# Kernel tuning notes

Hardware: AMD Instinct MI355X
Metric: run time of the kernel (lower is better)

## Reference

```python
import jax, jax.numpy as jnp
import numpy as np

D_MODEL = 768
KAN_HIDDEN = 2048
NUM_CP = 16        # number of B-spline control points / coefficients per edge
DEGREE = 3         # cubic splines
RMIN, RMAX = -4.0, 4.0


def bspline_basis(x, num_cp=NUM_CP, degree=DEGREE, rmin=RMIN, rmax=RMAX):
    """Cox-de Boor B-spline basis.
    x: (N, D) -> basis: (N, D, num_cp). Uniform knots extended by `degree`
    on each side so that [rmin, rmax] has full basis support.
    """
    h = (rmax - rmin) / (num_cp - degree)
    # K = num_cp + degree + 1 knots
    knots = rmin - degree * h + jnp.arange(num_cp + degree + 1, dtype=x.dtype) * h
    xe = x[..., None]  # (N, D, 1)
    # degree-0 indicator bases: (N, D, num_cp + degree)
    b = ((xe >= knots[:-1]) & (xe < knots[1:])).astype(x.dtype)
    for d in range(1, degree + 1):
        t0 = knots[:-(d + 1)]   # t[k]
        t1 = knots[d:-1]        # t[k+d]
        t2 = knots[d + 1:]      # t[k+d+1]
        t3 = knots[1:-d]        # t[k+1]
        b = (xe - t0) / (t1 - t0) * b[..., :-1] + (t2 - xe) / (t2 - t3) * b[..., 1:]
    return b  # (N, D, num_cp)


def kan_layer(x, w):
    """x: (N, Din); w: (Dout, Din, num_cp) per-edge spline coefficients."""
    basis = bspline_basis(x)                      # (N, Din, K)
    return jnp.einsum('ndk,odk->no', basis, w)    # (N, Dout)


def setup_inputs() -> dict:
    key = jax.random.key(0)
    kx, k1, k2 = jax.random.split(key, 3)
    x = jax.random.normal(kx, (2, 2048, D_MODEL), dtype=jnp.float32)
    # spline coefficient tables, small init like nn.init scaled normal
    w1 = jax.random.normal(k1, (KAN_HIDDEN, D_MODEL, NUM_CP), dtype=jnp.float32) * (1.0 / np.sqrt(D_MODEL * NUM_CP))
    w2 = jax.random.normal(k2, (D_MODEL, KAN_HIDDEN, NUM_CP), dtype=jnp.float32) * (1.0 / np.sqrt(KAN_HIDDEN * NUM_CP))
    return {"x": x, "w1": w1, "w2": w2}


def reference(x, w1, w2):
    B, T, D = x.shape
    input_dtype = x.dtype
    h = x.reshape(B * T, D).astype(jnp.float32)
    h = kan_layer(h, w1)                # (B*T, KAN_HIDDEN)
    h = kan_layer(h, w2)                # (B*T, D_MODEL)
    h = h.astype(input_dtype)
    # dropout p=0.0 / eval mode -> identity
    return h.reshape(B, T, -1)
```

## Files before the change

### kernel.cpp

```cpp
#include <hip/hip_runtime.h>
#include <stdint.h>

typedef __attribute__((ext_vector_type(8))) short short8;
typedef __attribute__((ext_vector_type(4))) float f32x4;
typedef __attribute__((ext_vector_type(4))) int i32x4;

#define DMODEL 768
#define HID    2048
#define MROWS  4096

#define KINVH  (13.0f/8.0f)
#define KNOT0  (-4.0f - 3.0f*(8.0f/13.0f))

__device__ __forceinline__ unsigned short f2bf(float f) {
  unsigned int u = __float_as_uint(f);
  unsigned int r = (u + 0x7FFFu + ((u >> 16) & 1u)) >> 16;
  return (unsigned short)r;
}

template<int DIN>
__global__ void __launch_bounds__(256) conv_pack(const float* __restrict__ src,
                                                 unsigned short* __restrict__ dst,
                                                 int total_waves) {
  constexpr int NK2 = DIN / 2;
  int gw = blockIdx.x * 4 + (threadIdx.x >> 6);
  if (gw >= total_waves) return;
  int l   = threadIdx.x & 63;
  int cb  = gw / NK2;
  int kt2 = gw % NK2;
  int c16 = l & 15, q = l >> 4;
  int col = cb * 16 + c16;
  const float* s = src + ((size_t)col * DIN + kt2 * 2 + (q >> 1)) * 16 + (q & 1) * 8;
  float4 v0 = *(const float4*)s;
  float4 v1 = *(const float4*)(s + 4);
  short8 o;
  o[0] = (short)f2bf(v0.x); o[1] = (short)f2bf(v0.y);
  o[2] = (short)f2bf(v0.z); o[3] = (short)f2bf(v0.w);
  o[4] = (short)f2bf(v1.x); o[5] = (short)f2bf(v1.y);
  o[6] = (short)f2bf(v1.z); o[7] = (short)f2bf(v1.w);
  unsigned short* d = dst + (((size_t)cb * NK2 + kt2) * 64 + q * 16 + c16) * 8;
  *(short8*)d = o;
}

__global__ void __launch_bounds__(256) reduce2(float4* __restrict__ p, int n4) {
  int i = blockIdx.x * 256 + threadIdx.x;
  if (i >= n4) return;
  float4 a = p[i], b = p[i + n4];
  float4 r;
  r.x = a.x + b.x; r.y = a.y + b.y; r.z = a.z + b.z; r.w = a.w + b.w;
  p[i] = r;
}

__global__ void __launch_bounds__(256) reduce4(const float4* __restrict__ p,
                                               float4* __restrict__ out, int n4) {
  int i = blockIdx.x * 256 + threadIdx.x;
  if (i >= n4) return;
  float4 a = p[i], b = p[i + n4], c = p[i + 2 * n4], d = p[i + 3 * n4];
  float4 r;
  r.x = a.x + b.x + c.x + d.x;
  r.y = a.y + b.y + c.y + d.y;
  r.z = a.z + b.z + c.z + d.z;
  r.w = a.w + b.w + c.w + d.w;
  out[i] = r;
}

template<int DIN, int DOUT, int SPLITK>
__global__ void __launch_bounds__(256, 4)
kan_gemm(const float* __restrict__ X, const unsigned short* __restrict__ Wb,
         float* __restrict__ Out) {
  constexpr int BM  = 64;
  constexpr int BN  = 256;
  constexpr int NK  = (DIN * 16) / 64;
  constexpr int NK2 = DIN / 2;
  constexpr int NKS = NK / SPLITK;
  constexpr int GX  = MROWS / BM;
  constexpr int GY  = DOUT / BN;
  constexpr int CPX = (GX * GY) / 8;
  __shared__ __align__(16) char smA[BM * 128];

  const int tid  = threadIdx.x;
  const int lane = tid & 63;
  const int wid  = tid >> 6;

  const int d    = blockIdx.x + blockIdx.y * GX;
  const int lf   = (d & 7) * CPX + (d >> 3);
  const int brow = (lf % GX) * BM;
  const int bcol = (lf / GX) * BN;
  const int kt0  = blockIdx.z * NKS;
  const int kt1  = kt0 + NKS;

  f32x4 acc[4][4];
#pragma unroll
  for (int m = 0; m < 4; ++m)
#pragma unroll
    for (int n = 0; n < 4; ++n) acc[m][n] = (f32x4){0.f, 0.f, 0.f, 0.f};

  int a_base[4], a_sw[4];
#pragma unroll
  for (int m = 0; m < 4; ++m) {
    int row   = m * 16 + (lane & 15);
    a_base[m] = row * 128 + ((lane >> 4) * 16);
    a_sw[m]   = (row & 7) << 4;
  }

  const unsigned short* bp[4];
#pragma unroll
  for (int n = 0; n < 4; ++n)
    bp[n] = Wb + ((size_t)(bcol / 16 + wid * 4 + n) * NK2 + (size_t)kt0 * 2) * 512
               + lane * 8;

  const int br_ = tid >> 2;
  const int bd_ = tid & 3;
  const float* xrow = X + (size_t)(brow + br_) * DIN + bd_;

  float xcur = xrow[(size_t)kt0 * 4];
  short8 bv[2][4];
#pragma unroll
  for (int n = 0; n < 4; ++n) {
    bv[0][n] = *(const short8*)(bp[n]);
    bv[1][n] = *(const short8*)(bp[n] + 512);
    bp[n] += 1024;
  }

  for (int kt = kt0; kt < kt1; ++kt) {
    __syncthreads();

    {
      float u  = (xcur - KNOT0) * KINVH;
      float uf = floorf(u);
      int   jj = (int)uf;
      float t  = u - uf;
      float t2 = t * t, t3 = t2 * t;
      float p0 = (1.0f / 6.0f) * (1.0f - 3.0f * t + 3.0f * t2 - t3);
      float p1 = (1.0f / 6.0f) * (4.0f - 6.0f * t2 + 3.0f * t3);
      float p2 = (1.0f / 6.0f) * (1.0f + 3.0f * t + 3.0f * t2 - 3.0f * t3);
      float p3 = (1.0f / 6.0f) * t3;

      int base = br_ * 128 + bd_ * 32;
      int sw   = (br_ & 7) << 4;
      *(i32x4*)(smA + (base ^ sw))        = (i32x4){0, 0, 0, 0};
      *(i32x4*)(smA + ((base + 16) ^ sw)) = (i32x4){0, 0, 0, 0};
      unsigned short q0 = f2bf(p0), q1 = f2bf(p1), q2 = f2bf(p2), q3 = f2bf(p3);
      int k0 = jj - 3;
      if ((unsigned)(k0 + 0) < 16u) *(unsigned short*)(smA + ((base + (k0 + 0) * 2) ^ sw)) = q0;
      if ((unsigned)(k0 + 1) < 16u) *(unsigned short*)(smA + ((base + (k0 + 1) * 2) ^ sw)) = q1;
      if ((unsigned)(k0 + 2) < 16u) *(unsigned short*)(smA + ((base + (k0 + 2) * 2) ^ sw)) = q2;
      if ((unsigned)(k0 + 3) < 16u) *(unsigned short*)(smA + ((base + (k0 + 3) * 2) ^ sw)) = q3;
    }

    {
      int ktn = (kt + 1 < kt1) ? kt + 1 : kt;
      xcur = xrow[(size_t)ktn * 4];
    }

    __syncthreads();

#pragma unroll
    for (int kk = 0; kk < 2; ++kk) {
      short8 a[4];
#pragma unroll
      for (int m = 0; m < 4; ++m)
        a[m] = *(const short8*)(smA + ((a_base[m] + kk * 64) ^ a_sw[m]));
#pragma unroll
      for (int m = 0; m < 4; ++m)
#pragma unroll
        for (int n = 0; n < 4; ++n)
          acc[m][n] = __builtin_amdgcn_mfma_f32_16x16x32_bf16(a[m], bv[kk][n], acc[m][n], 0, 0, 0);
    }

    if (kt + 1 < kt1) {
#pragma unroll
      for (int n = 0; n < 4; ++n) {
        bv[0][n] = *(const short8*)(bp[n]);
        bv[1][n] = *(const short8*)(bp[n] + 512);
        bp[n] += 1024;
      }
    }
  }

  float* outp = Out + (size_t)blockIdx.z * MROWS * DOUT;
#pragma unroll
  for (int m = 0; m < 4; ++m)
#pragma unroll
    for (int n = 0; n < 4; ++n)
#pragma unroll
      for (int q = 0; q < 4; ++q) {
        int grow = brow + m * 16 + (lane >> 4) * 4 + q;
        int gcol = bcol + wid * 64 + n * 16 + (lane & 15);
        outp[(size_t)grow * DOUT + gcol] = acc[m][n][q];
      }
}

extern "C" void kernel_launch(void* const* d_in, const int* in_sizes, int n_in,
                              void* d_out, int out_size, void* d_ws, size_t ws_size,
                              hipStream_t stream) {
  const float* x  = (const float*)d_in[0];
  const float* w1 = (const float*)d_in[1];
  const float* w2 = (const float*)d_in[2];
  float* out = (float*)d_out;

  char* ws = (char*)d_ws;
  unsigned short* wgb   = (unsigned short*)ws;
  float*          part1 = (float*)(ws + 50331648);
  float*          hbf   = part1;
  float*          part2 = (float*)(ws + 83886080);

  {
    const int waves = (HID / 16) * (DMODEL / 2);
    conv_pack<DMODEL><<<waves / 4, 256, 0, stream>>>(w1, wgb, waves);
  }
  kan_gemm<DMODEL, HID, 2>
      <<<dim3(MROWS / 64, HID / 256, 2), 256, 0, stream>>>(x, wgb, part1);
  const int hn4 = (MROWS * HID) / 4;
  reduce2<<<hn4 / 256, 256, 0, stream>>>((float4*)part1, hn4);

  {
    const int waves = (DMODEL / 16) * (HID / 2);
    conv_pack<HID><<<waves / 4, 256, 0, stream>>>(w2, wgb, waves);
  }
  kan_gemm<HID, DMODEL, 4>
      <<<dim3(MROWS / 64, DMODEL / 256, 4), 256, 0, stream>>>(hbf, wgb, part2);
  const int rn4 = (MROWS * DMODEL) / 4;
  reduce4<<<rn4 / 256, 256, 0, stream>>>((const float4*)part2, (float4*)out, rn4);
}
```

Before: 454.5 us.

## Fuse w2 packing with hidden reduce, narrow second GEMM tile, simplify basis math

Merges the w2 bf16 packing and the split-K reduction of the first layer into one launch, which removes a kernel launch and lets the two memory-bound jobs run side by side. The GEMM tile width becomes a template parameter, and the second layer now uses BN=128, doubling its grid to fill more CUs. The cubic B-spline weights are rewritten in the (1-t) form with fewer operations, and bf16 conversion now calls the HIP intrinsic. Narrower tiles reuse each A tile less, so more basis rebuilding and X reads happen per output.

```diff
diff --git a/kernel.cpp b/kernel.cpp
--- a/kernel.cpp
+++ b/kernel.cpp
@@ -1,4 +1,5 @@
 #include <hip/hip_runtime.h>
+#include <hip/hip_bf16.h>
 #include <stdint.h>
 
 typedef __attribute__((ext_vector_type(8))) short short8;
@@ -13,18 +14,14 @@
 #define KNOT0  (-4.0f - 3.0f*(8.0f/13.0f))
 
 __device__ __forceinline__ unsigned short f2bf(float f) {
-  unsigned int u = __float_as_uint(f);
-  unsigned int r = (u + 0x7FFFu + ((u >> 16) & 1u)) >> 16;
-  return (unsigned short)r;
+  __hip_bfloat16 h = __float2bfloat16(f);
+  return *reinterpret_cast<unsigned short*>(&h);
 }
 
 template<int DIN>
-__global__ void __launch_bounds__(256) conv_pack(const float* __restrict__ src,
-                                                 unsigned short* __restrict__ dst,
-                                                 int total_waves) {
+__device__ __forceinline__ void pack_wave(const float* __restrict__ src,
+                                          unsigned short* __restrict__ dst, int gw) {
   constexpr int NK2 = DIN / 2;
-  int gw = blockIdx.x * 4 + (threadIdx.x >> 6);
-  if (gw >= total_waves) return;
   int l   = threadIdx.x & 63;
   int cb  = gw / NK2;
   int kt2 = gw % NK2;
@@ -38,17 +35,30 @@
   o[2] = (short)f2bf(v0.z); o[3] = (short)f2bf(v0.w);
   o[4] = (short)f2bf(v1.x); o[5] = (short)f2bf(v1.y);
   o[6] = (short)f2bf(v1.z); o[7] = (short)f2bf(v1.w);
-  unsigned short* d = dst + (((size_t)cb * NK2 + kt2) * 64 + q * 16 + c16) * 8;
-  *(short8*)d = o;
-}
-
-__global__ void __launch_bounds__(256) reduce2(float4* __restrict__ p, int n4) {
-  int i = blockIdx.x * 256 + threadIdx.x;
-  if (i >= n4) return;
-  float4 a = p[i], b = p[i + n4];
-  float4 r;
-  r.x = a.x + b.x; r.y = a.y + b.y; r.z = a.z + b.z; r.w = a.w + b.w;
-  p[i] = r;
+  *(short8*)(dst + (((size_t)cb * NK2 + kt2) * 64 + q * 16 + c16) * 8) = o;
+}
+
+__global__ void __launch_bounds__(256) conv_pack1(const float* __restrict__ src,
+                                                  unsigned short* __restrict__ dst) {
+  pack_wave<DMODEL>(src, dst, blockIdx.x * 4 + (threadIdx.x >> 6));
+}
+
+__global__ void __launch_bounds__(256) pack2_reduce2(const float* __restrict__ w2,
+                                                     unsigned short* __restrict__ dst,
+                                                     float4* __restrict__ p, int n4) {
+  constexpr int PACK_BLOCKS = ((DMODEL / 16) * (HID / 2)) / 4;
+  int b = blockIdx.x;
+  if (b < PACK_BLOCKS) {
+    pack_wave<HID>(w2, dst, b * 4 + (threadIdx.x >> 6));
+  } else {
+    int i = (b - PACK_BLOCKS) * 256 + threadIdx.x;
+    if (i < n4) {
+      float4 a = p[i], q = p[i + n4];
+      float4 r;
+      r.x = a.x + q.x; r.y = a.y + q.y; r.z = a.z + q.z; r.w = a.w + q.w;
+      p[i] = r;
+    }
+  }
 }
 
 __global__ void __launch_bounds__(256) reduce4(const float4* __restrict__ p,
@@ -64,12 +74,12 @@
   out[i] = r;
 }
 
-template<int DIN, int DOUT, int SPLITK>
+template<int DIN, int DOUT, int BN, int SPLITK>
 __global__ void __launch_bounds__(256, 4)
 kan_gemm(const float* __restrict__ X, const unsigned short* __restrict__ Wb,
          float* __restrict__ Out) {
   constexpr int BM  = 64;
-  constexpr int BN  = 256;
+  constexpr int FN  = BN / 64;
   constexpr int NK  = (DIN * 16) / 64;
   constexpr int NK2 = DIN / 2;
   constexpr int NKS = NK / SPLITK;
@@ -89,11 +99,11 @@
   const int kt0  = blockIdx.z * NKS;
   const int kt1  = kt0 + NKS;
 
-  f32x4 acc[4][4];
+  f32x4 acc[4][FN];
 #pragma unroll
   for (int m = 0; m < 4; ++m)
 #pragma unroll
-    for (int n = 0; n < 4; ++n) acc[m][n] = (f32x4){0.f, 0.f, 0.f, 0.f};
+    for (int n = 0; n < FN; ++n) acc[m][n] = (f32x4){0.f, 0.f, 0.f, 0.f};
 
   int a_base[4], a_sw[4];
 #pragma unroll
@@ -103,10 +113,10 @@
     a_sw[m]   = (row & 7) << 4;
   }
 
-  const unsigned short* bp[4];
-#pragma unroll
-  for (int n = 0; n < 4; ++n)
-    bp[n] = Wb + ((size_t)(bcol / 16 + wid * 4 + n) * NK2 + (size_t)kt0 * 2) * 512
+  const unsigned short* bp[FN];
+#pragma unroll
+  for (int n = 0; n < FN; ++n)
+    bp[n] = Wb + ((size_t)(bcol / 16 + wid * FN + n) * NK2 + (size_t)kt0 * 2) * 512
                + lane * 8;
 
   const int br_ = tid >> 2;
@@ -114,9 +124,9 @@
   const float* xrow = X + (size_t)(brow + br_) * DIN + bd_;
 
   float xcur = xrow[(size_t)kt0 * 4];
-  short8 bv[2][4];
-#pragma unroll
-  for (int n = 0; n < 4; ++n) {
+  short8 bv[2][FN];
+#pragma unroll
+  for (int n = 0; n < FN; ++n) {
     bv[0][n] = *(const short8*)(bp[n]);
     bv[1][n] = *(const short8*)(bp[n] + 512);
     bp[n] += 1024;
@@ -130,11 +140,13 @@
       float uf = floorf(u);
       int   jj = (int)uf;
       float t  = u - uf;
+      float s1 = 1.0f - t;
       float t2 = t * t, t3 = t2 * t;
-      float p0 = (1.0f / 6.0f) * (1.0f - 3.0f * t + 3.0f * t2 - t3);
-      float p1 = (1.0f / 6.0f) * (4.0f - 6.0f * t2 + 3.0f * t3);
-      float p2 = (1.0f / 6.0f) * (1.0f + 3.0f * t + 3.0f * t2 - 3.0f * t3);
-      float p3 = (1.0f / 6.0f) * t3;
+      float s2 = s1 * s1, s3 = s2 * s1;
+      float p0 = s3 * (1.0f / 6.0f);
+      float p3 = t3 * (1.0f / 6.0f);
+      float p1 = fmaf(0.5f, t3, 2.0f / 3.0f) - t2;
+      float p2 = fmaf(0.5f, s3, 2.0f / 3.0f) - s2;
 
       int base = br_ * 128 + bd_ * 32;
       int sw   = (br_ & 7) << 4;
@@ -164,13 +176,13 @@
 #pragma unroll
       for (int m = 0; m < 4; ++m)
 #pragma unroll
-        for (int n = 0; n < 4; ++n)
+        for (int n = 0; n < FN; ++n)
           acc[m][n] = __builtin_amdgcn_mfma_f32_16x16x32_bf16(a[m], bv[kk][n], acc[m][n], 0, 0, 0);
     }
 
     if (kt + 1 < kt1) {
 #pragma unroll
-      for (int n = 0; n < 4; ++n) {
+      for (int n = 0; n < FN; ++n) {
         bv[0][n] = *(const short8*)(bp[n]);
         bv[1][n] = *(const short8*)(bp[n] + 512);
         bp[n] += 1024;
@@ -182,11 +194,11 @@
 #pragma unroll
   for (int m = 0; m < 4; ++m)
 #pragma unroll
-    for (int n = 0; n < 4; ++n)
+    for (int n = 0; n < FN; ++n)
 #pragma unroll
       for (int q = 0; q < 4; ++q) {
         int grow = brow + m * 16 + (lane >> 4) * 4 + q;
-        int gcol = bcol + wid * 64 + n * 16 + (lane & 15);
+        int gcol = bcol + wid * (BN / 4) + n * 16 + (lane & 15);
         outp[(size_t)grow * DOUT + gcol] = acc[m][n][q];
       }
 }
@@ -205,21 +217,18 @@
   float*          hbf   = part1;
   float*          part2 = (float*)(ws + 83886080);
 
+  conv_pack1<<<((HID / 16) * (DMODEL / 2)) / 4, 256, 0, stream>>>(w1, wgb);
+  kan_gemm<DMODEL, HID, 256, 2>
+      <<<dim3(MROWS / 64, HID / 256, 2), 256, 0, stream>>>(x, wgb, part1);
+
   {
-    const int waves = (HID / 16) * (DMODEL / 2);
-    conv_pack<DMODEL><<<waves / 4, 256, 0, stream>>>(w1, wgb, waves);
-  }
-  kan_gemm<DMODEL, HID, 2>
-      <<<dim3(MROWS / 64, HID / 256, 2), 256, 0, stream>>>(x, wgb, part1);
-  const int hn4 = (MROWS * HID) / 4;
-  reduce2<<<hn4 / 256, 256, 0, stream>>>((float4*)part1, hn4);
-
-  {
-    const int waves = (DMODEL / 16) * (HID / 2);
-    conv_pack<HID><<<waves / 4, 256, 0, stream>>>(w2, wgb, waves);
-  }
-  kan_gemm<HID, DMODEL, 4>
-      <<<dim3(MROWS / 64, DMODEL / 256, 4), 256, 0, stream>>>(hbf, wgb, part2);
+    const int hn4 = (MROWS * HID) / 4;
+    const int packB = ((DMODEL / 16) * (HID / 2)) / 4;
+    const int redB  = hn4 / 256;
+    pack2_reduce2<<<packB + redB, 256, 0, stream>>>(w2, wgb, (float4*)part1, hn4);
+  }
+  kan_gemm<HID, DMODEL, 128, 4>
+      <<<dim3(MROWS / 64, DMODEL / 128, 4), 256, 0, stream>>>(hbf, wgb, part2);
   const int rn4 = (MROWS * DMODEL) / 4;
   reduce4<<<rn4 / 256, 256, 0, stream>>>((const float4*)part2, (float4*)out, rn4);
 }
```

New measurement: 525.5 us. +15.6%, slower.
